# Kernel optimization log

Hardware: AMD Instinct MI355X
Metric: run time of the kernel (lower is better)

## Reference

```python
import jax, jax.numpy as jnp
import numpy as np

B, T, IN, OUT = 32, 1024, 1024, 1024
DT = 1.0
TAU_MIN, TAU_MAX = 5.0, 25.0


def setup_inputs() -> dict:
    key = jax.random.key(0)
    k1, k2, k3 = jax.random.split(key, 3)
    bound = 1.0 / np.sqrt(IN)
    inputs = jax.random.normal(k1, (B, T, IN), dtype=jnp.float32)
    weight = jax.random.uniform(k2, (OUT, IN), dtype=jnp.float32, minval=-bound, maxval=bound)
    bias = jnp.zeros((OUT,), dtype=jnp.float32)
    # per-neuron decay alpha = exp(-dt/tau), tau ~ U[tau_min, tau_max]
    tau = jax.random.uniform(k3, (OUT,), dtype=jnp.float32, minval=TAU_MIN, maxval=TAU_MAX)
    decay = jnp.exp(-DT / tau)
    return {"inputs": inputs, "weight": weight, "bias": bias, "decay": decay}


def reference(inputs, weight, bias, decay):
    # time-distributed linear projection: [B,T,IN] @ [OUT,IN]^T -> [B,T,OUT]
    current = jnp.einsum('bti,oi->bto', inputs, weight) + bias
    u0 = jnp.zeros((inputs.shape[0], weight.shape[0]), dtype=current.dtype)

    def step(u, x_t):
        # leaky integrator: u_t = alpha*u_{t-1} + (1-alpha)*x_t
        u = decay * u + (1.0 - decay) * x_t
        return u, u

    # scan over time: move T to leading axis
    _, u_seq = jax.lax.scan(step, u0, jnp.swapaxes(current, 0, 1))
    return jnp.swapaxes(u_seq, 0, 1)  # [B,T,OUT]
```

## Files before the change

kernel.cpp:

```cpp
#include <hip/hip_runtime.h>

#define M_DIM 32768
#define N_DIM 1024
#define K_DIM 1024
#define T_DIM 1024
#define B_DIM 32
#define NCHUNK 8
#define CHUNK_T 128

typedef unsigned int uint32;
typedef __attribute__((ext_vector_type(8))) short short8;
typedef __attribute__((ext_vector_type(8))) unsigned short ushort8v;
typedef __attribute__((ext_vector_type(4))) float floatx4;

__device__ __forceinline__ unsigned short f2bf(float f) {
    uint32 u = __float_as_uint(f);
    uint32 r = u + 0x7fffu + ((u >> 16) & 1u);
    return (unsigned short)(r >> 16);
}

__device__ __forceinline__ void async_load16(const void* g, void* s) {
    __builtin_amdgcn_global_load_lds(
        (const __attribute__((address_space(1))) void*)g,
        (__attribute__((address_space(3))) void*)s,
        16, 0, 0);
}

__global__ void cast_f32_bf16_x8(const float* __restrict__ src,
                                 unsigned short* __restrict__ dst, int n8) {
    int i = blockIdx.x * blockDim.x + threadIdx.x;
    if (i < n8) {
        const float4* s4 = (const float4*)src;
        float4 v0 = s4[(size_t)i * 2];
        float4 v1 = s4[(size_t)i * 2 + 1];
        ushort8v o;
        o[0] = f2bf(v0.x); o[1] = f2bf(v0.y); o[2] = f2bf(v0.z); o[3] = f2bf(v0.w);
        o[4] = f2bf(v1.x); o[5] = f2bf(v1.y); o[6] = f2bf(v1.z); o[7] = f2bf(v1.w);
        ((ushort8v*)dst)[i] = o;
    }
}

__global__ __launch_bounds__(512, 2) void gemm_8phase(
    const unsigned short* __restrict__ A,
    const unsigned short* __restrict__ Bw,
    const float* __restrict__ bias,
    unsigned short* __restrict__ outBf) {
    extern __shared__ __align__(16) unsigned short smem[];

    const int tid  = threadIdx.x;
    const int lane = tid & 63;
    const int wid  = tid >> 6;
    const int l15  = lane & 15;
    const int quad = lane >> 4;
    const int wm   = wid >> 2;
    const int wn   = wid & 3;

    const int L   = blockIdx.y * gridDim.x + blockIdx.x;
    const int xcd = L & 7;
    const int s   = L >> 3;
    const int bn0 = (s & 3) * 256;
    const int bm0 = (xcd * 16 + (s >> 2)) * 256;

    const int t3  = tid >> 3;
    const int sc8 = ((tid & 7) ^ (t3 & 7)) * 8;

#define STAGE_A(IH, T, PB) do {                                              \
        size_t kof_ = (size_t)(T) * 64 + sc8;                                \
        _Pragma("unroll") for (int q_ = 0; q_ < 2; ++q_) {                   \
            int ar_ = q_ * 128 + (IH) * 64 + t3;                             \
            int dr_ = q_ * 128 + (IH) * 64 + wid * 8;                        \
            async_load16(A + (size_t)(bm0 + ar_) * K_DIM + kof_,             \
                         smem + (PB) * 32768 + dr_ * 64);                    \
        } } while (0)
#define STAGE_B(JH, T, PB) do {                                              \
        size_t kof_ = (size_t)(T) * 64 + sc8;                                \
        _Pragma("unroll") for (int q_ = 0; q_ < 2; ++q_) {                   \
            int br_ = (q_ * 2 + (tid >> 8)) * 64 + (JH) * 32 + (t3 & 31);    \
            int dr_ = (q_ * 2 + (wid >> 2)) * 64 + (JH) * 32 + (wid & 3) * 8;\
            async_load16(Bw + (size_t)(bn0 + br_) * K_DIM + kof_,            \
                         smem + (PB) * 32768 + 16384 + dr_ * 64);            \
        } } while (0)

#define LD_A(IH) do {                                                        \
        const unsigned short* As_ = smem + pb * 32768;                       \
        _Pragma("unroll") for (int ii = 0; ii < 4; ++ii) {                   \
            int r_ = wm * 128 + (IH) * 64 + ii * 16 + l15;                   \
            _Pragma("unroll") for (int ks = 0; ks < 2; ++ks) {               \
                int c_ = ks * 4 + quad;                                      \
                af[ii][ks] = *(const short8*)&As_[r_ * 64 +                  \
                                                 ((c_ ^ (l15 & 7)) * 8)];    \
            } } } while (0)
#define LD_B(JH) do {                                                        \
        const unsigned short* Bs_ = smem + pb * 32768 + 16384;               \
        _Pragma("unroll") for (int jj = 0; jj < 2; ++jj) {                   \
            int r_ = wn * 64 + ((JH) * 2 + jj) * 16 + l15;                   \
            _Pragma("unroll") for (int ks = 0; ks < 2; ++ks) {               \
                int c_ = ks * 4 + quad;                                      \
                bfr[(JH) * 2 + jj][ks] = *(const short8*)&Bs_[r_ * 64 +      \
                                                 ((c_ ^ (l15 & 7)) * 8)];    \
            } } } while (0)
#define MM(IH, JH) do {                                                      \
        __builtin_amdgcn_s_setprio(1);                                       \
        _Pragma("unroll") for (int ii = 0; ii < 4; ++ii)                     \
        _Pragma("unroll") for (int jj = 0; jj < 2; ++jj)                     \
        _Pragma("unroll") for (int ks = 0; ks < 2; ++ks)                     \
            acc[(IH) * 4 + ii][(JH) * 2 + jj] =                              \
                __builtin_amdgcn_mfma_f32_16x16x32_bf16(                     \
                    af[ii][ks], bfr[(JH) * 2 + jj][ks],                      \
                    acc[(IH) * 4 + ii][(JH) * 2 + jj], 0, 0, 0);             \
        __builtin_amdgcn_s_setprio(0);                                       \
    } while (0)

#define FENCE  asm volatile("" ::: "memory")
#define BAR    __builtin_amdgcn_s_barrier()
#define LGKM0  asm volatile("s_waitcnt lgkmcnt(0)" ::: "memory")
#define SCHED0 __builtin_amdgcn_sched_barrier(0)

    floatx4 acc[8][4];
#pragma unroll
    for (int i = 0; i < 8; ++i)
#pragma unroll
        for (int j = 0; j < 4; ++j)
            acc[i][j] = (floatx4){0.f, 0.f, 0.f, 0.f};

    short8 af[4][2];
    short8 bfr[4][2];

    const int NT = K_DIM / 64;

    STAGE_A(0, 0, 0); STAGE_A(1, 0, 0); STAGE_B(0, 0, 0); STAGE_B(1, 0, 0);
    STAGE_A(0, 1, 1); STAGE_B(1, 1, 1); STAGE_B(0, 1, 1);
    asm volatile("s_waitcnt vmcnt(6)" ::: "memory");
    FENCE; BAR;

    for (int g = 0; g < NT; ++g) {
        const int pb = g & 1;
        const int po = pb ^ 1;

        LD_A(0); LD_B(0);
        if (g + 1 < NT) STAGE_A(1, g + 1, po);
        FENCE; BAR; LGKM0; SCHED0;
        MM(0, 0);
        SCHED0; FENCE; BAR;

        LD_B(1);
        if (g + 2 < NT) STAGE_A(0, g + 2, pb);
        FENCE; BAR; LGKM0; SCHED0;
        MM(0, 1);
        SCHED0; FENCE; BAR;

        LD_A(1);
        if (g + 2 < NT) STAGE_B(1, g + 2, pb);
        FENCE; BAR; LGKM0; SCHED0;
        MM(1, 0);
        SCHED0; FENCE; BAR;

        if (g + 2 < NT) STAGE_B(0, g + 2, pb);
        if (g < NT - 2) {
            asm volatile("s_waitcnt vmcnt(6)" ::: "memory");
        } else if (g == NT - 2) {
            asm volatile("s_waitcnt vmcnt(0)" ::: "memory");
        }
        FENCE; BAR; LGKM0; SCHED0;
        MM(1, 1);
        SCHED0; FENCE; BAR;
    }
    asm volatile("s_waitcnt vmcnt(0)" ::: "memory");

    float bb[4];
#pragma unroll
    for (int j = 0; j < 4; ++j) bb[j] = bias[bn0 + wn * 64 + j * 16 + l15];
#pragma unroll
    for (int i = 0; i < 8; ++i) {
        int rowb = bm0 + wm * 128 + i * 16 + quad * 4;
#pragma unroll
        for (int r = 0; r < 4; ++r) {
            size_t rb = (size_t)(rowb + r) * N_DIM + bn0 + wn * 64 + l15;
#pragma unroll
            for (int j = 0; j < 4; ++j)
                outBf[rb + j * 16] = f2bf(acc[i][j][r] + bb[j]);
        }
    }
#undef STAGE_A
#undef STAGE_B
#undef LD_A
#undef LD_B
#undef MM
#undef FENCE
#undef BAR
#undef LGKM0
#undef SCHED0
}

__global__ __launch_bounds__(256) void gemm_mfma(
    const unsigned short* __restrict__ A,
    const unsigned short* __restrict__ Bw,
    const float* __restrict__ bias,
    unsigned short* outBf,
    float* outF) {
    __shared__ unsigned short As[128 * 64];
    __shared__ unsigned short Bs[128 * 64];

    const int tid  = threadIdx.x;
    const int lane = tid & 63;
    const int wid  = tid >> 6;
    const int l15  = lane & 15;
    const int quad = lane >> 4;
    const int wm   = wid >> 1;
    const int wn   = wid & 1;

    const int L    = blockIdx.y * gridDim.x + blockIdx.x;
    const int xcd  = L & 7;
    const int s    = L >> 3;
    const int bn0  = (s & 7) * 128;
    const int bm0  = (xcd * 32 + (s >> 3)) * 128;

    floatx4 acc[4][4];
#pragma unroll
    for (int i = 0; i < 4; ++i)
#pragma unroll
        for (int j = 0; j < 4; ++j)
            acc[i][j] = (floatx4){0.f, 0.f, 0.f, 0.f};

    for (int kt = 0; kt < K_DIM / 64; ++kt) {
        const int k0 = kt * 64;
#pragma unroll
        for (int q = 0; q < 4; ++q) {
            int slot = q * 256 + tid;
            int row  = slot >> 3;
            int chq  = slot & 7;
            int scq  = chq ^ (row & 7);
            async_load16(A + (size_t)(bm0 + row) * K_DIM + k0 + scq * 8,
                         &As[(q * 256 + wid * 64) * 8]);
        }
#pragma unroll
        for (int q = 0; q < 4; ++q) {
            int slot = q * 256 + tid;
            int row  = slot >> 3;
            int chq  = slot & 7;
            int scq  = chq ^ (row & 7);
            async_load16(Bw + (size_t)(bn0 + row) * K_DIM + k0 + scq * 8,
                         &Bs[(q * 256 + wid * 64) * 8]);
        }
        __syncthreads();

#pragma unroll
        for (int ks = 0; ks < 2; ++ks) {
            short8 af[4], bfr[4];
#pragma unroll
            for (int i = 0; i < 4; ++i) {
                int r = wm * 64 + i * 16 + l15;
                int c = ks * 4 + quad;
                af[i] = *(const short8*)&As[r * 64 + ((c ^ (r & 7)) * 8)];
            }
#pragma unroll
            for (int j = 0; j < 4; ++j) {
                int r = wn * 64 + j * 16 + l15;
                int c = ks * 4 + quad;
                bfr[j] = *(const short8*)&Bs[r * 64 + ((c ^ (r & 7)) * 8)];
            }
#pragma unroll
            for (int i = 0; i < 4; ++i)
#pragma unroll
                for (int j = 0; j < 4; ++j)
                    acc[i][j] = __builtin_amdgcn_mfma_f32_16x16x32_bf16(
                        af[i], bfr[j], acc[i][j], 0, 0, 0);
        }
        __syncthreads();
    }

#pragma unroll
    for (int j = 0; j < 4; ++j) {
        int col = bn0 + wn * 64 + j * 16 + l15;
        float bb = bias[col];
#pragma unroll
        for (int i = 0; i < 4; ++i) {
            int rowb = bm0 + wm * 64 + i * 16 + quad * 4;
#pragma unroll
            for (int r = 0; r < 4; ++r) {
                float v = acc[i][j][r] + bb;
                size_t idx = (size_t)(rowb + r) * N_DIM + col;
                if (outBf) outBf[idx] = f2bf(v);
                else       outF[idx]  = v;
            }
        }
    }
}

__global__ __launch_bounds__(256) void scan_carry2(
    const uint32* __restrict__ cur32,
    const float* __restrict__ decay,
    float* __restrict__ carry) {
    int tid   = blockIdx.x * 256 + threadIdx.x;
    int o2    = tid & 511;
    int chunk = (tid >> 9) & (NCHUNK - 1);
    int b     = tid >> 12;
    int o     = o2 * 2;
    size_t base = ((size_t)b * T_DIM + (size_t)chunk * CHUNK_T) * (N_DIM / 2) + o2;
    float2 a2 = *(const float2*)&decay[o];
    float a0 = a2.x, a1 = a2.y;
    float c0 = 1.f - a0, c1 = 1.f - a1;
    float u0 = 0.f, u1 = 0.f;
    for (int t0 = 0; t0 < CHUNK_T; t0 += 32) {
        uint32 x[32];
#pragma unroll
        for (int k = 0; k < 32; ++k)
            x[k] = cur32[base + (size_t)(t0 + k) * (N_DIM / 2)];
#pragma unroll
        for (int k = 0; k < 32; ++k) {
            float lo = __uint_as_float(x[k] << 16);
            float hi = __uint_as_float(x[k] & 0xffff0000u);
            u0 = a0 * u0 + c0 * lo;
            u1 = a1 * u1 + c1 * hi;
        }
    }
    float2* cw = (float2*)&carry[((size_t)b * NCHUNK + chunk) * N_DIM + o];
    *cw = (float2){u0, u1};
}

__global__ __launch_bounds__(256) void scan_apply2(
    const uint32* __restrict__ cur32,
    const float* __restrict__ decay,
    const float* __restrict__ carry,
    float* __restrict__ out) {
    int tid   = blockIdx.x * 256 + threadIdx.x;
    int o2    = tid & 511;
    int chunk = (tid >> 9) & (NCHUNK - 1);
    int b     = tid >> 12;
    int o     = o2 * 2;
    size_t base = ((size_t)b * T_DIM + (size_t)chunk * CHUNK_T) * (N_DIM / 2) + o2;
    float2 a2 = *(const float2*)&decay[o];
    float a0 = a2.x, a1 = a2.y;
    float c0 = 1.f - a0, c1 = 1.f - a1;

    float A0 = a0, A1 = a1;
#pragma unroll
    for (int i = 0; i < 7; ++i) { A0 *= A0; A1 *= A1; }

    float u0 = 0.f, u1 = 0.f;
    const float* cb = carry + (size_t)b * NCHUNK * N_DIM + o;
    for (int i = 0; i < chunk; ++i) {
        float2 cv = *(const float2*)&cb[(size_t)i * N_DIM];
        u0 = cv.x + A0 * u0;
        u1 = cv.y + A1 * u1;
    }

    float2* out2 = (float2*)out;
    size_t obase = ((size_t)b * T_DIM + (size_t)chunk * CHUNK_T) * (N_DIM / 2) + o2;
    for (int t0 = 0; t0 < CHUNK_T; t0 += 32) {
        uint32 x[32];
#pragma unroll
        for (int k = 0; k < 32; ++k)
            x[k] = cur32[base + (size_t)(t0 + k) * (N_DIM / 2)];
#pragma unroll
        for (int k = 0; k < 32; ++k) {
            float lo = __uint_as_float(x[k] << 16);
            float hi = __uint_as_float(x[k] & 0xffff0000u);
            u0 = a0 * u0 + c0 * lo;
            u1 = a1 * u1 + c1 * hi;
            out2[obase + (size_t)(t0 + k) * (N_DIM / 2)] = (float2){u0, u1};
        }
    }
}

__global__ void scan_f32_inplace(float* __restrict__ buf,
                                 const float* __restrict__ decay) {
    int tid = blockIdx.x * 64 + threadIdx.x;
    int o = tid & (N_DIM - 1);
    size_t base = ((size_t)(tid >> 10) << 20) + o;
    float a = decay[o];
    float c = 1.f - a;
    float u = 0.f;
    for (int t0 = 0; t0 < 1024; t0 += 16) {
        float x[16];
#pragma unroll
        for (int k = 0; k < 16; ++k)
            x[k] = buf[base + (size_t)(t0 + k) * N_DIM];
#pragma unroll
        for (int k = 0; k < 16; ++k) {
            u = a * u + c * x[k];
            buf[base + (size_t)(t0 + k) * N_DIM] = u;
        }
    }
}

__global__ void gemm_naive(const float* __restrict__ X, const float* __restrict__ W,
                           const float* __restrict__ bias, float* __restrict__ out) {
    __shared__ float As[16][17], Bs[16][17];
    int tx = threadIdx.x, ty = threadIdx.y;
    int m0 = blockIdx.y * 16, n0 = blockIdx.x * 16;
    float acc = 0.f;
    for (int k0 = 0; k0 < K_DIM; k0 += 16) {
        As[ty][tx] = X[(size_t)(m0 + ty) * K_DIM + k0 + tx];
        Bs[ty][tx] = W[(size_t)(n0 + ty) * K_DIM + k0 + tx];
        __syncthreads();
#pragma unroll
        for (int kk = 0; kk < 16; ++kk) acc += As[ty][kk] * Bs[tx][kk];
        __syncthreads();
    }
    out[(size_t)(m0 + ty) * N_DIM + n0 + tx] = acc + bias[n0 + tx];
}

extern "C" void kernel_launch(void* const* d_in, const int* in_sizes, int n_in,
                              void* d_out, int out_size, void* d_ws, size_t ws_size,
                              hipStream_t stream) {
    const float* X     = (const float*)d_in[0];
    const float* Wt    = (const float*)d_in[1];
    const float* bias  = (const float*)d_in[2];
    const float* decay = (const float*)d_in[3];
    float* out = (float*)d_out;

    static bool big_lds_ok = [] {
        return hipFuncSetAttribute(reinterpret_cast<const void*>(gemm_8phase),
                                   hipFuncAttributeMaxDynamicSharedMemorySize,
                                   131072) == hipSuccess;
    }();

    const size_t A_bytes  = (size_t)M_DIM * K_DIM * 2;
    const size_t W_bytes  = (size_t)N_DIM * K_DIM * 2;
    const size_t C_bytes  = (size_t)M_DIM * N_DIM * 2;
    const size_t cr_bytes = (size_t)B_DIM * NCHUNK * N_DIM * 4;
    const size_t need_mid  = A_bytes + W_bytes;
    const size_t need_full = A_bytes + W_bytes + C_bytes + cr_bytes;

    if (ws_size >= need_full) {
        unsigned short* Abf = (unsigned short*)d_ws;
        unsigned short* Wbf = (unsigned short*)((char*)d_ws + A_bytes);
        unsigned short* Cbf = (unsigned short*)((char*)d_ws + A_bytes + W_bytes);
        float* carry = (float*)((char*)d_ws + A_bytes + W_bytes + C_bytes);
        cast_f32_bf16_x8<<<(M_DIM * K_DIM / 8 + 255) / 256, 256, 0, stream>>>(X, Abf, M_DIM * K_DIM / 8);
        cast_f32_bf16_x8<<<(N_DIM * K_DIM / 8 + 255) / 256, 256, 0, stream>>>(Wt, Wbf, N_DIM * K_DIM / 8);
        if (big_lds_ok) {
            gemm_8phase<<<dim3(4, 128), 512, 131072, stream>>>(Abf, Wbf, bias, Cbf);
        } else {
            gemm_mfma<<<dim3(N_DIM / 128, M_DIM / 128), 256, 0, stream>>>(Abf, Wbf, bias, Cbf, nullptr);
        }
        const int scan_threads = B_DIM * NCHUNK * N_DIM / 2;
        scan_carry2<<<scan_threads / 256, 256, 0, stream>>>((const uint32*)Cbf, decay, carry);
        scan_apply2<<<scan_threads / 256, 256, 0, stream>>>((const uint32*)Cbf, decay, carry, out);
    } else if (ws_size >= need_mid) {
        unsigned short* Abf = (unsigned short*)d_ws;
        unsigned short* Wbf = (unsigned short*)((char*)d_ws + A_bytes);
        cast_f32_bf16_x8<<<(M_DIM * K_DIM / 8 + 255) / 256, 256, 0, stream>>>(X, Abf, M_DIM * K_DIM / 8);
        cast_f32_bf16_x8<<<(N_DIM * K_DIM / 8 + 255) / 256, 256, 0, stream>>>(Wt, Wbf, N_DIM * K_DIM / 8);
        gemm_mfma<<<dim3(N_DIM / 128, M_DIM / 128), 256, 0, stream>>>(Abf, Wbf, bias, nullptr, out);
        scan_f32_inplace<<<512, 64, 0, stream>>>(out, decay);
    } else {
        gemm_naive<<<dim3(N_DIM / 16, M_DIM / 16), dim3(16, 16), 0, stream>>>(X, Wt, bias, out);
        scan_f32_inplace<<<512, 64, 0, stream>>>(out, decay);
    }
}
```

Measured before the change: 154.9 us.

## Fuse per-chunk scan carry computation into GEMM epilogue

The GEMM epilogue now computes each 128-timestep chunk's decayed sum directly from the fp32 accumulators. It weights each row by a power of decay, reduces across lanes with shuffles, and writes the chunk carry. This removes the separate scan_carry2 kernel, which reread the whole bf16 intermediate from memory. The epilogue gets extra arithmetic and register pressure. The carry is now computed from fp32 values instead of rounded bf16 values, which changes numerics slightly.

```diff
diff --git a/kernel.cpp b/kernel.cpp
--- a/kernel.cpp
+++ b/kernel.cpp
@@ -25,6 +25,50 @@
         (__attribute__((address_space(3))) void*)s,
         16, 0, 0);
 }
+
+#define FENCE  asm volatile("" ::: "memory")
+#define BAR    __builtin_amdgcn_s_barrier()
+#define LGKM0  asm volatile("s_waitcnt lgkmcnt(0)" ::: "memory")
+#define SCHED0 __builtin_amdgcn_sched_barrier(0)
+
+#define STAGE_B(JH, T, PB) do {                                              \
+        size_t kof_ = (size_t)(T) * 64 + sc8;                                \
+        _Pragma("unroll") for (int q_ = 0; q_ < 2; ++q_) {                   \
+            int br_ = (q_ * 2 + (tid >> 8)) * 64 + (JH) * 32 + (t3 & 31);    \
+            int dr_ = (q_ * 2 + (wid >> 2)) * 64 + (JH) * 32 + (wid & 3) * 8;\
+            async_load16(Bw + (size_t)(bn0 + br_) * K_DIM + kof_,            \
+                         smem + (PB) * 32768 + 16384 + dr_ * 64);            \
+        } } while (0)
+
+#define LD_A8(IH) do {                                                       \
+        const unsigned short* As_ = smem + pb * 32768;                       \
+        _Pragma("unroll") for (int ii = 0; ii < 4; ++ii) {                   \
+            int r_ = wm * 128 + (IH) * 64 + ii * 16 + l15;                   \
+            _Pragma("unroll") for (int ks = 0; ks < 2; ++ks) {               \
+                int c_ = ks * 4 + quad;                                      \
+                af[ii][ks] = *(const short8*)&As_[r_ * 64 +                  \
+                                                 ((c_ ^ (l15 & 7)) * 8)];    \
+            } } } while (0)
+#define LD_B8(JH) do {                                                       \
+        const unsigned short* Bs_ = smem + pb * 32768 + 16384;               \
+        _Pragma("unroll") for (int jj = 0; jj < 2; ++jj) {                   \
+            int r_ = wn * 64 + ((JH) * 2 + jj) * 16 + l15;                   \
+            _Pragma("unroll") for (int ks = 0; ks < 2; ++ks) {               \
+                int c_ = ks * 4 + quad;                                      \
+                bfr[(JH) * 2 + jj][ks] = *(const short8*)&Bs_[r_ * 64 +      \
+                                                 ((c_ ^ (l15 & 7)) * 8)];    \
+            } } } while (0)
+#define MM8(IH, JH) do {                                                     \
+        __builtin_amdgcn_s_setprio(1);                                       \
+        _Pragma("unroll") for (int ii = 0; ii < 4; ++ii)                     \
+        _Pragma("unroll") for (int jj = 0; jj < 2; ++jj)                     \
+        _Pragma("unroll") for (int ks = 0; ks < 2; ++ks)                     \
+            acc[(IH) * 4 + ii][(JH) * 2 + jj] =                              \
+                __builtin_amdgcn_mfma_f32_16x16x32_bf16(                     \
+                    af[ii][ks], bfr[(JH) * 2 + jj][ks],                      \
+                    acc[(IH) * 4 + ii][(JH) * 2 + jj], 0, 0, 0);             \
+        __builtin_amdgcn_s_setprio(0);                                       \
+    } while (0)
 
 __global__ void cast_f32_bf16_x8(const float* __restrict__ src,
                                  unsigned short* __restrict__ dst, int n8) {
@@ -44,7 +88,9 @@
     const unsigned short* __restrict__ A,
     const unsigned short* __restrict__ Bw,
     const float* __restrict__ bias,
-    unsigned short* __restrict__ outBf) {
+    const float* __restrict__ decay,
+    unsigned short* __restrict__ outBf,
+    float* __restrict__ carry) {
     extern __shared__ __align__(16) unsigned short smem[];
 
     const int tid  = threadIdx.x;
@@ -72,49 +118,6 @@
             async_load16(A + (size_t)(bm0 + ar_) * K_DIM + kof_,             \
                          smem + (PB) * 32768 + dr_ * 64);                    \
         } } while (0)
-#define STAGE_B(JH, T, PB) do {                                              \
-        size_t kof_ = (size_t)(T) * 64 + sc8;                                \
-        _Pragma("unroll") for (int q_ = 0; q_ < 2; ++q_) {                   \
-            int br_ = (q_ * 2 + (tid >> 8)) * 64 + (JH) * 32 + (t3 & 31);    \
-            int dr_ = (q_ * 2 + (wid >> 2)) * 64 + (JH) * 32 + (wid & 3) * 8;\
-            async_load16(Bw + (size_t)(bn0 + br_) * K_DIM + kof_,            \
-                         smem + (PB) * 32768 + 16384 + dr_ * 64);            \
-        } } while (0)
-
-#define LD_A(IH) do {                                                        \
-        const unsigned short* As_ = smem + pb * 32768;                       \
-        _Pragma("unroll") for (int ii = 0; ii < 4; ++ii) {                   \
-            int r_ = wm * 128 + (IH) * 64 + ii * 16 + l15;                   \
-            _Pragma("unroll") for (int ks = 0; ks < 2; ++ks) {               \
-                int c_ = ks * 4 + quad;                                      \
-                af[ii][ks] = *(const short8*)&As_[r_ * 64 +                  \
-                                                 ((c_ ^ (l15 & 7)) * 8)];    \
-            } } } while (0)
-#define LD_B(JH) do {                                                        \
-        const unsigned short* Bs_ = smem + pb * 32768 + 16384;               \
-        _Pragma("unroll") for (int jj = 0; jj < 2; ++jj) {                   \
-            int r_ = wn * 64 + ((JH) * 2 + jj) * 16 + l15;                   \
-            _Pragma("unroll") for (int ks = 0; ks < 2; ++ks) {               \
-                int c_ = ks * 4 + quad;                                      \
-                bfr[(JH) * 2 + jj][ks] = *(const short8*)&Bs_[r_ * 64 +      \
-                                                 ((c_ ^ (l15 & 7)) * 8)];    \
-            } } } while (0)
-#define MM(IH, JH) do {                                                      \
-        __builtin_amdgcn_s_setprio(1);                                       \
-        _Pragma("unroll") for (int ii = 0; ii < 4; ++ii)                     \
-        _Pragma("unroll") for (int jj = 0; jj < 2; ++jj)                     \
-        _Pragma("unroll") for (int ks = 0; ks < 2; ++ks)                     \
-            acc[(IH) * 4 + ii][(JH) * 2 + jj] =                              \
-                __builtin_amdgcn_mfma_f32_16x16x32_bf16(                     \
-                    af[ii][ks], bfr[(JH) * 2 + jj][ks],                      \
-                    acc[(IH) * 4 + ii][(JH) * 2 + jj], 0, 0, 0);             \
-        __builtin_amdgcn_s_setprio(0);                                       \
-    } while (0)
-
-#define FENCE  asm volatile("" ::: "memory")
-#define BAR    __builtin_amdgcn_s_barrier()
-#define LGKM0  asm volatile("s_waitcnt lgkmcnt(0)" ::: "memory")
-#define SCHED0 __builtin_amdgcn_sched_barrier(0)
 
     floatx4 acc[8][4];
 #pragma unroll
@@ -137,22 +140,22 @@
         const int pb = g & 1;
         const int po = pb ^ 1;
 
-        LD_A(0); LD_B(0);
+        LD_A8(0); LD_B8(0);
         if (g + 1 < NT) STAGE_A(1, g + 1, po);
         FENCE; BAR; LGKM0; SCHED0;
-        MM(0, 0);
+        MM8(0, 0);
         SCHED0; FENCE; BAR;
 
-        LD_B(1);
+        LD_B8(1);
         if (g + 2 < NT) STAGE_A(0, g + 2, pb);
         FENCE; BAR; LGKM0; SCHED0;
-        MM(0, 1);
+        MM8(0, 1);
         SCHED0; FENCE; BAR;
 
-        LD_A(1);
+        LD_A8(1);
         if (g + 2 < NT) STAGE_B(1, g + 2, pb);
         FENCE; BAR; LGKM0; SCHED0;
-        MM(1, 0);
+        MM8(1, 0);
         SCHED0; FENCE; BAR;
 
         if (g + 2 < NT) STAGE_B(0, g + 2, pb);
@@ -162,7 +165,7 @@
             asm volatile("s_waitcnt vmcnt(0)" ::: "memory");
         }
         FENCE; BAR; LGKM0; SCHED0;
-        MM(1, 1);
+        MM8(1, 1);
         SCHED0; FENCE; BAR;
     }
     asm volatile("s_waitcnt vmcnt(0)" ::: "memory");
@@ -181,141 +184,38 @@
                 outBf[rb + j * 16] = f2bf(acc[i][j][r] + bb[j]);
         }
     }
+
+    {
+        const int q4 = quad * 4;
+        const int bchk = ((bm0 >> 10) * NCHUNK) + ((bm0 >> 7) & 7) + wm;
+        float* cdst = carry + (size_t)bchk * N_DIM + bn0 + wn * 64;
+#pragma unroll
+        for (int j = 0; j < 4; ++j) {
+            float a  = decay[bn0 + wn * 64 + j * 16 + l15];
+            float a2 = a * a, a4 = a2 * a2, a8 = a4 * a4, a16 = a8 * a8;
+            float S = 0.f;
+#pragma unroll
+            for (int r = 0; r < 4; ++r) {
+                int n = 15 - q4 - r;
+                float w = 1.f;
+                w *= (n & 1) ? a  : 1.f;
+                w *= (n & 2) ? a2 : 1.f;
+                w *= (n & 4) ? a4 : 1.f;
+                w *= (n & 8) ? a8 : 1.f;
+#pragma unroll
+                for (int ii = 0; ii < 8; ++ii) {
+                    S = fmaf(w, acc[7 - ii][j][r], S);
+                    w *= a16;
+                }
+            }
+            S += __shfl_xor(S, 16, 64);
+            S += __shfl_xor(S, 32, 64);
+            float a32 = a16 * a16, a64 = a32 * a32, a128 = a64 * a64;
+            float cv = (1.f - a) * S + bb[j] * (1.f - a128);
+            if (quad == 0) cdst[j * 16 + l15] = cv;
+        }
+    }
 #undef STAGE_A
-#undef STAGE_B
-#undef LD_A
-#undef LD_B
-#undef MM
-#undef FENCE
-#undef BAR
-#undef LGKM0
-#undef SCHED0
-}
-
-__global__ __launch_bounds__(256) void gemm_mfma(
-    const unsigned short* __restrict__ A,
-    const unsigned short* __restrict__ Bw,
-    const float* __restrict__ bias,
-    unsigned short* outBf,
-    float* outF) {
-    __shared__ unsigned short As[128 * 64];
-    __shared__ unsigned short Bs[128 * 64];
-
-    const int tid  = threadIdx.x;
-    const int lane = tid & 63;
-    const int wid  = tid >> 6;
-    const int l15  = lane & 15;
-    const int quad = lane >> 4;
-    const int wm   = wid >> 1;
-    const int wn   = wid & 1;
-
-    const int L    = blockIdx.y * gridDim.x + blockIdx.x;
-    const int xcd  = L & 7;
-    const int s    = L >> 3;
-    const int bn0  = (s & 7) * 128;
-    const int bm0  = (xcd * 32 + (s >> 3)) * 128;
-
-    floatx4 acc[4][4];
-#pragma unroll
-    for (int i = 0; i < 4; ++i)
-#pragma unroll
-        for (int j = 0; j < 4; ++j)
-            acc[i][j] = (floatx4){0.f, 0.f, 0.f, 0.f};
-
-    for (int kt = 0; kt < K_DIM / 64; ++kt) {
-        const int k0 = kt * 64;
-#pragma unroll
-        for (int q = 0; q < 4; ++q) {
-            int slot = q * 256 + tid;
-            int row  = slot >> 3;
-            int chq  = slot & 7;
-            int scq  = chq ^ (row & 7);
-            async_load16(A + (size_t)(bm0 + row) * K_DIM + k0 + scq * 8,
-                         &As[(q * 256 + wid * 64) * 8]);
-        }
-#pragma unroll
-        for (int q = 0; q < 4; ++q) {
-            int slot = q * 256 + tid;
-            int row  = slot >> 3;
-            int chq  = slot & 7;
-            int scq  = chq ^ (row & 7);
-            async_load16(Bw + (size_t)(bn0 + row) * K_DIM + k0 + scq * 8,
-                         &Bs[(q * 256 + wid * 64) * 8]);
-        }
-        __syncthreads();
-
-#pragma unroll
-        for (int ks = 0; ks < 2; ++ks) {
-            short8 af[4], bfr[4];
-#pragma unroll
-            for (int i = 0; i < 4; ++i) {
-                int r = wm * 64 + i * 16 + l15;
-                int c = ks * 4 + quad;
-                af[i] = *(const short8*)&As[r * 64 + ((c ^ (r & 7)) * 8)];
-            }
-#pragma unroll
-            for (int j = 0; j < 4; ++j) {
-                int r = wn * 64 + j * 16 + l15;
-                int c = ks * 4 + quad;
-                bfr[j] = *(const short8*)&Bs[r * 64 + ((c ^ (r & 7)) * 8)];
-            }
-#pragma unroll
-            for (int i = 0; i < 4; ++i)
-#pragma unroll
-                for (int j = 0; j < 4; ++j)
-                    acc[i][j] = __builtin_amdgcn_mfma_f32_16x16x32_bf16(
-                        af[i], bfr[j], acc[i][j], 0, 0, 0);
-        }
-        __syncthreads();
-    }
-
-#pragma unroll
-    for (int j = 0; j < 4; ++j) {
-        int col = bn0 + wn * 64 + j * 16 + l15;
-        float bb = bias[col];
-#pragma unroll
-        for (int i = 0; i < 4; ++i) {
-            int rowb = bm0 + wm * 64 + i * 16 + quad * 4;
-#pragma unroll
-            for (int r = 0; r < 4; ++r) {
-                float v = acc[i][j][r] + bb;
-                size_t idx = (size_t)(rowb + r) * N_DIM + col;
-                if (outBf) outBf[idx] = f2bf(v);
-                else       outF[idx]  = v;
-            }
-        }
-    }
-}
-
-__global__ __launch_bounds__(256) void scan_carry2(
-    const uint32* __restrict__ cur32,
-    const float* __restrict__ decay,
-    float* __restrict__ carry) {
-    int tid   = blockIdx.x * 256 + threadIdx.x;
-    int o2    = tid & 511;
-    int chunk = (tid >> 9) & (NCHUNK - 1);
-    int b     = tid >> 12;
-    int o     = o2 * 2;
-    size_t base = ((size_t)b * T_DIM + (size_t)chunk * CHUNK_T) * (N_DIM / 2) + o2;
-    float2 a2 = *(const float2*)&decay[o];
-    float a0 = a2.x, a1 = a2.y;
-    float c0 = 1.f - a0, c1 = 1.f - a1;
-    float u0 = 0.f, u1 = 0.f;
-    for (int t0 = 0; t0 < CHUNK_T; t0 += 32) {
-        uint32 x[32];
-#pragma unroll
-        for (int k = 0; k < 32; ++k)
-            x[k] = cur32[base + (size_t)(t0 + k) * (N_DIM / 2)];
-#pragma unroll
-        for (int k = 0; k < 32; ++k) {
-            float lo = __uint_as_float(x[k] << 16);
-            float hi = __uint_as_float(x[k] & 0xffff0000u);
-            u0 = a0 * u0 + c0 * lo;
-            u1 = a1 * u1 + c1 * hi;
-        }
-    }
-    float2* cw = (float2*)&carry[((size_t)b * NCHUNK + chunk) * N_DIM + o];
-    *cw = (float2){u0, u1};
 }
 
 __global__ __launch_bounds__(256) void scan_apply2(
@@ -384,6 +284,101 @@
     }
 }
 
+__global__ __launch_bounds__(256) void gemm_mfma(
+    const unsigned short* __restrict__ A,
+    const unsigned short* __restrict__ Bw,
+    const float* __restrict__ bias,
+    unsigned short* outBf,
+    float* outF) {
+    __shared__ unsigned short As[128 * 64];
+    __shared__ unsigned short Bs[128 * 64];
+
+    const int tid  = threadIdx.x;
+    const int lane = tid & 63;
+    const int wid  = tid >> 6;
+    const int l15  = lane & 15;
+    const int quad = lane >> 4;
+    const int wm   = wid >> 1;
+    const int wn   = wid & 1;
+
+    const int L    = blockIdx.y * gridDim.x + blockIdx.x;
+    const int xcd  = L & 7;
+    const int s    = L >> 3;
+    const int bn0  = (s & 7) * 128;
+    const int bm0  = (xcd * 32 + (s >> 3)) * 128;
+
+    floatx4 acc[4][4];
+#pragma unroll
+    for (int i = 0; i < 4; ++i)
+#pragma unroll
+        for (int j = 0; j < 4; ++j)
+            acc[i][j] = (floatx4){0.f, 0.f, 0.f, 0.f};
+
+    for (int kt = 0; kt < K_DIM / 64; ++kt) {
+        const int k0 = kt * 64;
+#pragma unroll
+        for (int q = 0; q < 4; ++q) {
+            int slot = q * 256 + tid;
+            int row  = slot >> 3;
+            int chq  = slot & 7;
+            int scq  = chq ^ (row & 7);
+            async_load16(A + (size_t)(bm0 + row) * K_DIM + k0 + scq * 8,
+                         &As[(q * 256 + wid * 64) * 8]);
+        }
+#pragma unroll
+        for (int q = 0; q < 4; ++q) {
+            int slot = q * 256 + tid;
+            int row  = slot >> 3;
+            int chq  = slot & 7;
+            int scq  = chq ^ (row & 7);
+            async_load16(Bw + (size_t)(bn0 + row) * K_DIM + k0 + scq * 8,
+                         &Bs[(q * 256 + wid * 64) * 8]);
+        }
+        __syncthreads();
+
+#pragma unroll
+        for (int ks = 0; ks < 2; ++ks) {
+            short8 af[4], bfr[4];
+#pragma unroll
+            for (int i = 0; i < 4; ++i) {
+                int r = wm * 64 + i * 16 + l15;
+                int c = ks * 4 + quad;
+                af[i] = *(const short8*)&As[r * 64 + ((c ^ (r & 7)) * 8)];
+            }
+#pragma unroll
+            for (int j = 0; j < 4; ++j) {
+                int r = wn * 64 + j * 16 + l15;
+                int c = ks * 4 + quad;
+                bfr[j] = *(const short8*)&Bs[r * 64 + ((c ^ (r & 7)) * 8)];
+            }
+#pragma unroll
+            for (int i = 0; i < 4; ++i)
+#pragma unroll
+                for (int j = 0; j < 4; ++j)
+                    acc[i][j] = __builtin_amdgcn_mfma_f32_16x16x32_bf16(
+                        af[i], bfr[j], acc[i][j], 0, 0, 0);
+        }
+        __syncthreads();
+    }
+
+#pragma unroll
+    for (int j = 0; j < 4; ++j) {
+        int col = bn0 + wn * 64 + j * 16 + l15;
+        float bb = bias[col];
+#pragma unroll
+        for (int i = 0; i < 4; ++i) {
+            int rowb = bm0 + wm * 64 + i * 16 + quad * 4;
+#pragma unroll
+            for (int r = 0; r < 4; ++r) {
+                float v = acc[i][j][r] + bb;
+                size_t idx = (size_t)(rowb + r) * N_DIM + col;
+                if (outBf) outBf[idx] = f2bf(v);
+                else       outF[idx]  = v;
+            }
+        }
+    }
+}
+
 __global__ void gemm_naive(const float* __restrict__ X, const float* __restrict__ W,
                            const float* __restrict__ bias, float* __restrict__ out) {
     __shared__ float As[16][17], Bs[16][17];
@@ -410,7 +405,7 @@
     const float* decay = (const float*)d_in[3];
     float* out = (float*)d_out;
 
-    static bool big_lds_ok = [] {
+    static bool lds128_ok = [] {
         return hipFuncSetAttribute(reinterpret_cast<const void*>(gemm_8phase),
                                    hipFuncAttributeMaxDynamicSharedMemorySize,
                                    131072) == hipSuccess;
@@ -422,21 +417,16 @@
     const size_t cr_bytes = (size_t)B_DIM * NCHUNK * N_DIM * 4;
     const size_t need_mid  = A_bytes + W_bytes;
     const size_t need_full = A_bytes + W_bytes + C_bytes + cr_bytes;
-
-    if (ws_size >= need_full) {
+    const int scan_threads = B_DIM * NCHUNK * N_DIM / 2;
+
+    if (lds128_ok && ws_size >= need_full) {
         unsigned short* Abf = (unsigned short*)d_ws;
         unsigned short* Wbf = (unsigned short*)((char*)d_ws + A_bytes);
         unsigned short* Cbf = (unsigned short*)((char*)d_ws + A_bytes + W_bytes);
         float* carry = (float*)((char*)d_ws + A_bytes + W_bytes + C_bytes);
         cast_f32_bf16_x8<<<(M_DIM * K_DIM / 8 + 255) / 256, 256, 0, stream>>>(X, Abf, M_DIM * K_DIM / 8);
         cast_f32_bf16_x8<<<(N_DIM * K_DIM / 8 + 255) / 256, 256, 0, stream>>>(Wt, Wbf, N_DIM * K_DIM / 8);
-        if (big_lds_ok) {
-            gemm_8phase<<<dim3(4, 128), 512, 131072, stream>>>(Abf, Wbf, bias, Cbf);
-        } else {
-            gemm_mfma<<<dim3(N_DIM / 128, M_DIM / 128), 256, 0, stream>>>(Abf, Wbf, bias, Cbf, nullptr);
-        }
-        const int scan_threads = B_DIM * NCHUNK * N_DIM / 2;
-        scan_carry2<<<scan_threads / 256, 256, 0, stream>>>((const uint32*)Cbf, decay, carry);
+        gemm_8phase<<<dim3(4, 128), 512, 131072, stream>>>(Abf, Wbf, bias, decay, Cbf, carry);
         scan_apply2<<<scan_threads / 256, 256, 0, stream>>>((const uint32*)Cbf, decay, carry, out);
     } else if (ws_size >= need_mid) {
         unsigned short* Abf = (unsigned short*)d_ws;
```

Measured after the change: 149.1 us. -3.8%, faster.
